# Performance work log

Measured on AMD Instinct MI355X. Metric: run time of the kernel, lower is better.

Reference implementation:

```python
import jax, jax.numpy as jnp
import numpy as np

B = 131072
# join branch layer dims: 203 -> 175 -> 150 -> 128 -> 80 -> 48
DIMS = [203, 175, 150, 128, 80, 48]

def setup_inputs() -> dict:
    key = jax.random.key(0)
    ks = jax.random.split(key, 11)
    inp = {"x": jax.random.normal(ks[0], (B, DIMS[0]), dtype=jnp.float32)}
    for i in range(5):
        fan_in, fan_out = DIMS[i], DIMS[i + 1]
        bound = 1.0 / np.sqrt(fan_in)
        inp[f"W{i+1}"] = jax.random.uniform(ks[1 + 2 * i], (fan_out, fan_in), minval=-bound, maxval=bound, dtype=jnp.float32)
        inp[f"b{i+1}"] = jax.random.uniform(ks[2 + 2 * i], (fan_out,), minval=-bound, maxval=bound, dtype=jnp.float32)
    return inp

def reference(x, W1, b1, W2, b2, W3, b3, W4, b4, W5, b5):
    # join branch of NodeEmbedding, dropout in eval mode (identity).
    h = jnp.tanh(x @ W1.T + b1)      # [B,175]
    h = jnp.tanh(h @ W2.T + b2)      # [B,150]
    h = jnp.tanh(h @ W3.T + b3)      # [B,128]
    h = jnp.tanh(h @ W4.T + b4)      # [B,80]
    return h @ W5.T + b5             # [B,48], no activation on last layer
```

## Files before the change

kernel.cpp:

```cpp
#include <hip/hip_runtime.h>


typedef short short8 __attribute__((ext_vector_type(8)));
typedef float f32x16 __attribute__((ext_vector_type(16)));
typedef unsigned int uint;
typedef unsigned short ushort;

#define SROW 180
#define XROW 212
#define NTHREADS 384

__device__ __forceinline__ ushort f2bf(float f) {
    uint u = __float_as_uint(f);
    u += 0x7FFFu + ((u >> 16) & 1u);
    return (ushort)(u >> 16);
}
__device__ __forceinline__ float bf2f(ushort h) { return __uint_as_float(((uint)h) << 16); }
__device__ __forceinline__ float fast_tanh(float x) {
    float e = __expf(2.0f * x);
    return 1.0f - 2.0f / (e + 1.0f);
}
__device__ __forceinline__ uint rbf(float v) {
    uint u = __float_as_uint(v);
    return u + 0x7FFFu + ((u >> 16) & 1u);
}

union U4S8 { uint4 u; short8 s; };

__global__ void prep_weights(const float* __restrict__ W1, const float* __restrict__ W2,
                             const float* __restrict__ W3, const float* __restrict__ W4,
                             const float* __restrict__ W5, char* __restrict__ ws)
{
    const int b = blockIdx.x, l = threadIdx.x;
    int layer, local;
    if      (b <  78) { layer = 0; local = b; }
    else if (b < 133) { layer = 1; local = b - 78; }
    else if (b < 173) { layer = 2; local = b - 133; }
    else if (b < 197) { layer = 3; local = b - 173; }
    else              { layer = 4; local = b - 197; }
    const int NTa[5]  = {6, 5, 4, 3, 2};
    const int FINa[5] = {203, 175, 150, 128, 80};
    const int FOa[5]  = {175, 150, 128, 80, 48};
    const float* Wp = (layer == 0) ? W1 : (layer == 1) ? W2 : (layer == 2) ? W3
                    : (layer == 3) ? W4 : W5;
    const int nt = NTa[layer], fin = FINa[layer], fout = FOa[layer];
    const int c = local / nt, t = local % nt;
    const int n  = t * 32 + (l & 31);
    const int kb = c * 16 + (l >> 5) * 8;
    uint hw[4], lw[4];
#pragma unroll
    for (int j = 0; j < 8; ++j) {
        int k = kb + j;
        float v = (n < fout && k < fin) ? Wp[(size_t)n * fin + k] : 0.0f;
        ushort hh = f2bf(v);
        ushort ll = f2bf(v - bf2f(hh));
        if (j & 1) { hw[j >> 1] |= ((uint)hh) << 16; lw[j >> 1] |= ((uint)ll) << 16; }
        else       { hw[j >> 1]  = hh;               lw[j >> 1]  = ll; }
    }
    char* dst = ws + (size_t)b * 2048 + l * 16;
    *(uint4*)dst          = make_uint4(hw[0], hw[1], hw[2], hw[3]);
    *(uint4*)(dst + 1024) = make_uint4(lw[0], lw[1], lw[2], lw[3]);
}

template<int KC, int NT, int FOUT, int PADN, int SR, bool ACT, bool LAST>
__device__ __forceinline__ void run_layer(const char* __restrict__ wsL,
    const float* __restrict__ bias, const uint* aP, uint* oP, float* outg,
    int row0, int l, int w, int lx, int lh, int tid)
{
    f32x16 acc;
    {
        float bv = 0.0f;
        if (w < NT) { int n = w * 32 + lx; bv = (n < FOUT) ? bias[n] : 0.0f; }
#pragma unroll
        for (int r = 0; r < 16; ++r) acc[r] = bv;
    }

    if (w < NT) {
#pragma unroll
        for (int c = 0; c < KC; ++c) {
            const uint4* wp = (const uint4*)wsL + (size_t)((c * NT + w) * 2) * 64 + l;
            U4S8 bh, bl;
            bh.u = wp[0];
            bl.u = wp[64];
            const uint* ap = aP + lx * SR + c * 16 + lh * 8;
            uint4 d0 = *(const uint4*)ap;
            uint4 d1 = *(const uint4*)(ap + 4);
            uint dd[8] = {d0.x, d0.y, d0.z, d0.w, d1.x, d1.y, d1.z, d1.w};
            U4S8 ah, al;
            uint* aHu = (uint*)&ah; uint* aLu = (uint*)&al;
#pragma unroll
            for (int j = 0; j < 4; ++j) {
                aHu[j] = (dd[2*j] >> 16)     | (dd[2*j + 1] & 0xFFFF0000u);
                aLu[j] = (dd[2*j] & 0xFFFFu) | (dd[2*j + 1] << 16);
            }
            acc = __builtin_amdgcn_mfma_f32_32x32x16_bf16(ah.s, bh.s, acc, 0, 0, 0);
            acc = __builtin_amdgcn_mfma_f32_32x32x16_bf16(al.s, bh.s, acc, 0, 0, 0);
            acc = __builtin_amdgcn_mfma_f32_32x32x16_bf16(ah.s, bl.s, acc, 0, 0, 0);
        }
    }
    if (!LAST) __syncthreads();

    if (w < NT) {
#pragma unroll
        for (int r = 0; r < 16; ++r) {
            float vv = acc[r];
            if (ACT) vv = fast_tanh(vv);
            int rowl = (r & 3) + 8 * (r >> 2) + 4 * lh;
            int col  = w * 32 + lx;
            if (LAST) {
                if (col < 48) outg[(size_t)(row0 + rowl) * 48 + col] = vv;
            } else if (col < FOUT) {
                uint r1  = rbf(vv);
                uint hib = r1 & 0xFFFF0000u;
                float lo = vv - __uint_as_float(hib);
                uint r2  = rbf(lo);
                oP[rowl * SROW + col] = hib | (r2 >> 16);
            }
        }
    }
    if (!LAST) {
        if (PADN > 0) {
            for (int idx = tid; idx < 32 * PADN; idx += NTHREADS) {
                int row = idx / PADN, p = idx % PADN;
                oP[row * SROW + FOUT + p] = 0u;
            }
        }
        __syncthreads();
    }
}

__global__ __launch_bounds__(NTHREADS, 5)
void mlp_mfma(const float* __restrict__ x,
              const float* __restrict__ b1, const float* __restrict__ b2,
              const float* __restrict__ b3, const float* __restrict__ b4,
              const float* __restrict__ b5,
              const char* __restrict__ ws, float* __restrict__ out)
{
    __shared__ __align__(16) uint buf[32 * XROW];

    const int tid = threadIdx.x;
    const int l = tid & 63, w = tid >> 6;
    const int lx = l & 31, lh = l >> 5;
    const int row0 = blockIdx.x * 32;

    for (int e = tid; e < 32 * 208; e += NTHREADS) {
        int row = e / 208, col = e - row * 208;
        float v = 0.0f;
        if (col < 203) v = x[(size_t)(row0 + row) * 203 + col];
        uint r1  = rbf(v);
        uint hib = r1 & 0xFFFF0000u;
        float lo = v - __uint_as_float(hib);
        uint r2  = rbf(lo);
        buf[row * XROW + col] = hib | (r2 >> 16);
    }
    __syncthreads();

    run_layer<13, 6, 175,  1, XROW, true,  false>(ws,             b1, buf, buf, nullptr, row0, l, w, lx, lh, tid);
    run_layer<11, 5, 150, 10, SROW, true,  false>(ws +  78 * 2048, b2, buf, buf, nullptr, row0, l, w, lx, lh, tid);
    run_layer<10, 4, 128,  0, SROW, true,  false>(ws + 133 * 2048, b3, buf, buf, nullptr, row0, l, w, lx, lh, tid);
    run_layer< 8, 3,  80,  0, SROW, true,  false>(ws + 173 * 2048, b4, buf, buf, nullptr, row0, l, w, lx, lh, tid);
    run_layer< 5, 2,  48,  0, SROW, false, true >(ws + 197 * 2048, b5, buf, buf, out,     row0, l, w, lx, lh, tid);
}

extern "C" void kernel_launch(void* const* d_in, const int* in_sizes, int n_in,
                              void* d_out, int out_size, void* d_ws, size_t ws_size,
                              hipStream_t stream) {
    (void)in_sizes; (void)n_in; (void)ws_size; (void)out_size;
    const float* x  = (const float*)d_in[0];
    const float* W1 = (const float*)d_in[1];
    const float* b1 = (const float*)d_in[2];
    const float* W2 = (const float*)d_in[3];
    const float* b2 = (const float*)d_in[4];
    const float* W3 = (const float*)d_in[5];
    const float* b3 = (const float*)d_in[6];
    const float* W4 = (const float*)d_in[7];
    const float* b4 = (const float*)d_in[8];
    const float* W5 = (const float*)d_in[9];
    const float* b5 = (const float*)d_in[10];
    float* out = (float*)d_out;
    char* ws = (char*)d_ws;

    hipLaunchKernelGGL(prep_weights, dim3(207), dim3(64), 0, stream,
                       W1, W2, W3, W4, W5, ws);
    hipLaunchKernelGGL(mlp_mfma, dim3(131072 / 32), dim3(NTHREADS), 0, stream,
                       x, b1, b2, b3, b4, b5, ws, out);
}
```

Baseline: 326.9 us.

## Split LDS activations into separate bf16 hi and lo planes

Activations in shared memory were stored as packed hi|lo 32-bit words, and each lane had to unpack them into hi and lo bf16 vectors with shifts and masks before every MFMA. They are now kept in two separate bf16 arrays, so each lane loads an MFMA operand directly with one 16-byte read per plane. This removes the per-chunk unpack ALU work and halves the LDS footprint per row (232 ushort stride per plane). In exchange, the epilogue does two 16-bit stores per element instead of one 32-bit store, and bank-conflict behaviour changes with the new stride.

```diff
diff --git a/kernel.cpp b/kernel.cpp
--- a/kernel.cpp
+++ b/kernel.cpp
@@ -6,8 +6,8 @@
 typedef unsigned int uint;
 typedef unsigned short ushort;
 
-#define SROW 180
-#define XROW 212
+#define PSTR 116
+#define PSTRU (PSTR*2)
 #define NTHREADS 384
 
 __device__ __forceinline__ ushort f2bf(float f) {
@@ -62,9 +62,9 @@
     *(uint4*)(dst + 1024) = make_uint4(lw[0], lw[1], lw[2], lw[3]);
 }
 
-template<int KC, int NT, int FOUT, int PADN, int SR, bool ACT, bool LAST>
+template<int KC, int NT, int FOUT, int PADN, bool ACT, bool LAST>
 __device__ __forceinline__ void run_layer(const char* __restrict__ wsL,
-    const float* __restrict__ bias, const uint* aP, uint* oP, float* outg,
+    const float* __restrict__ bias, uint* aH, uint* aL, float* outg,
     int row0, int l, int w, int lx, int lh, int tid)
 {
     f32x16 acc;
@@ -76,23 +76,16 @@
     }
 
     if (w < NT) {
+        const char* ha = (const char*)aH + lx * (PSTR * 4) + lh * 16;
+        const char* la = (const char*)aL + lx * (PSTR * 4) + lh * 16;
 #pragma unroll
         for (int c = 0; c < KC; ++c) {
             const uint4* wp = (const uint4*)wsL + (size_t)((c * NT + w) * 2) * 64 + l;
-            U4S8 bh, bl;
+            U4S8 bh, bl, ah, al;
             bh.u = wp[0];
             bl.u = wp[64];
-            const uint* ap = aP + lx * SR + c * 16 + lh * 8;
-            uint4 d0 = *(const uint4*)ap;
-            uint4 d1 = *(const uint4*)(ap + 4);
-            uint dd[8] = {d0.x, d0.y, d0.z, d0.w, d1.x, d1.y, d1.z, d1.w};
-            U4S8 ah, al;
-            uint* aHu = (uint*)&ah; uint* aLu = (uint*)&al;
-#pragma unroll
-            for (int j = 0; j < 4; ++j) {
-                aHu[j] = (dd[2*j] >> 16)     | (dd[2*j + 1] & 0xFFFF0000u);
-                aLu[j] = (dd[2*j] & 0xFFFFu) | (dd[2*j + 1] << 16);
-            }
+            ah.u = *(const uint4*)(ha + c * 32);
+            al.u = *(const uint4*)(la + c * 32);
             acc = __builtin_amdgcn_mfma_f32_32x32x16_bf16(ah.s, bh.s, acc, 0, 0, 0);
             acc = __builtin_amdgcn_mfma_f32_32x32x16_bf16(al.s, bh.s, acc, 0, 0, 0);
             acc = __builtin_amdgcn_mfma_f32_32x32x16_bf16(ah.s, bl.s, acc, 0, 0, 0);
@@ -101,6 +94,8 @@
     if (!LAST) __syncthreads();
 
     if (w < NT) {
+        ushort* pH = (ushort*)aH;
+        ushort* pL = (ushort*)aL;
 #pragma unroll
         for (int r = 0; r < 16; ++r) {
             float vv = acc[r];
@@ -114,15 +109,19 @@
                 uint hib = r1 & 0xFFFF0000u;
                 float lo = vv - __uint_as_float(hib);
                 uint r2  = rbf(lo);
-                oP[rowl * SROW + col] = hib | (r2 >> 16);
+                pH[rowl * PSTRU + col] = (ushort)(r1 >> 16);
+                pL[rowl * PSTRU + col] = (ushort)(r2 >> 16);
             }
         }
     }
     if (!LAST) {
         if (PADN > 0) {
+            ushort* pH = (ushort*)aH;
+            ushort* pL = (ushort*)aL;
             for (int idx = tid; idx < 32 * PADN; idx += NTHREADS) {
                 int row = idx / PADN, p = idx % PADN;
-                oP[row * SROW + FOUT + p] = 0u;
+                pH[row * PSTRU + FOUT + p] = 0;
+                pL[row * PSTRU + FOUT + p] = 0;
             }
         }
         __syncthreads();
@@ -136,30 +135,35 @@
               const float* __restrict__ b5,
               const char* __restrict__ ws, float* __restrict__ out)
 {
-    __shared__ __align__(16) uint buf[32 * XROW];
+    __shared__ __align__(16) uint aH[32 * PSTR];
+    __shared__ __align__(16) uint aL[32 * PSTR];
 
     const int tid = threadIdx.x;
     const int l = tid & 63, w = tid >> 6;
     const int lx = l & 31, lh = l >> 5;
     const int row0 = blockIdx.x * 32;
 
-    for (int e = tid; e < 32 * 208; e += NTHREADS) {
-        int row = e / 208, col = e - row * 208;
-        float v = 0.0f;
-        if (col < 203) v = x[(size_t)(row0 + row) * 203 + col];
-        uint r1  = rbf(v);
-        uint hib = r1 & 0xFFFF0000u;
-        float lo = v - __uint_as_float(hib);
-        uint r2  = rbf(lo);
-        buf[row * XROW + col] = hib | (r2 >> 16);
+    {
+        ushort* pH = (ushort*)aH;
+        ushort* pL = (ushort*)aL;
+        for (int e = tid; e < 32 * 208; e += NTHREADS) {
+            int row = e / 208, col = e - row * 208;
+            float v = (col < 203) ? x[(size_t)(row0 + row) * 203 + col] : 0.0f;
+            uint r1  = rbf(v);
+            uint hib = r1 & 0xFFFF0000u;
+            float lo = v - __uint_as_float(hib);
+            uint r2  = rbf(lo);
+            pH[row * PSTRU + col] = (ushort)(r1 >> 16);
+            pL[row * PSTRU + col] = (ushort)(r2 >> 16);
+        }
     }
     __syncthreads();
 
-    run_layer<13, 6, 175,  1, XROW, true,  false>(ws,             b1, buf, buf, nullptr, row0, l, w, lx, lh, tid);
-    run_layer<11, 5, 150, 10, SROW, true,  false>(ws +  78 * 2048, b2, buf, buf, nullptr, row0, l, w, lx, lh, tid);
-    run_layer<10, 4, 128,  0, SROW, true,  false>(ws + 133 * 2048, b3, buf, buf, nullptr, row0, l, w, lx, lh, tid);
-    run_layer< 8, 3,  80,  0, SROW, true,  false>(ws + 173 * 2048, b4, buf, buf, nullptr, row0, l, w, lx, lh, tid);
-    run_layer< 5, 2,  48,  0, SROW, false, true >(ws + 197 * 2048, b5, buf, buf, out,     row0, l, w, lx, lh, tid);
+    run_layer<13, 6, 175,  1, true,  false>(ws,              b1, aH, aL, nullptr, row0, l, w, lx, lh, tid);
+    run_layer<11, 5, 150, 10, true,  false>(ws +  78 * 2048, b2, aH, aL, nullptr, row0, l, w, lx, lh, tid);
+    run_layer<10, 4, 128,  0, true,  false>(ws + 133 * 2048, b3, aH, aL, nullptr, row0, l, w, lx, lh, tid);
+    run_layer< 8, 3,  80,  0, true,  false>(ws + 173 * 2048, b4, aH, aL, nullptr, row0, l, w, lx, lh, tid);
+    run_layer< 5, 2,  48,  0, false, true >(ws + 197 * 2048, b5, aH, aL, out,     row0, l, w, lx, lh, tid);
 }
 
 extern "C" void kernel_launch(void* const* d_in, const int* in_sizes, int n_in,
```

Result: faster. 311.9 us (-4.6%).
